# Kernel tuning notes

Measured on AMD Instinct MI355X. Metric: run time of the kernel, lower is better.

The kernel has to match this reference:

```python
import jax, jax.numpy as jnp
import numpy as np

MARGIN = 0.1
REDUCTION = 'mean'  # 'mean' or 'sum'

def setup_inputs() -> dict:
    key = jax.random.key(0)
    k1, k2 = jax.random.split(key)
    B, N = 16384, 64
    scores = jax.random.normal(k1, (B * N,), dtype=jnp.float32)
    werRank = jax.random.randint(k2, (B, N), 0, N, dtype=jnp.int64)
    return {"scores": scores, "werRank": werRank, "n_best": N}

def reference(scores, werRank, n_best):
    B = werRank.shape[0]
    N = n_best
    s = scores.reshape(B, N)                      # [B, N] per-utterance n-best scores
    g = jnp.take_along_axis(s, werRank, axis=1)   # [B, N] scores ordered by WER rank (best first)
    # pairwise margin: d[b, i, j] = g[b, j] - g[b, i] + margin, for worse-ranked j > i
    d = g[:, None, :] - g[:, :, None] + MARGIN    # [B, N, N]
    upper = jnp.triu(jnp.ones((N, N), dtype=bool), k=1)  # j > i
    hinge = jnp.where(upper[None], jnp.maximum(d, 0.0), 0.0)
    per_i = hinge.sum(axis=2)                     # [B, N] sum over worse hypotheses j
    if REDUCTION == 'mean':
        counts = (N - 1) - jnp.arange(N)          # len(nBestRank[i+1:]) for each i
        denom = jnp.where(counts > 0, counts, 1).astype(per_i.dtype)
        per_i = per_i / denom[None, :]            # row i=N-1 contributes 0 (skipped in original)
    return per_i.sum()
```

## Files before the change

### kernel.cpp

```cpp
#include <hip/hip_runtime.h>

#define MARGIN 0.1f
#define NBEST 64

__global__ __launch_bounds__(256)
void sml_kernel(const float* __restrict__ scores,
                const unsigned int* __restrict__ wr32,
                float* __restrict__ ws, int B)
{
    const int lane = threadIdx.x & 63;
    const int wib  = threadIdx.x >> 6;
    const int wgl  = blockIdx.x * 4 + wib;
    const int b0   = wgl * 4;

    unsigned int probe = wr32[2 * lane + 1];
    const bool is64 = (__all(probe == 0u) != 0);

    __shared__ float4 g4[4][NBEST];

    float gv[4];
    #pragma unroll
    for (int r = 0; r < 4; ++r) {
        int b  = b0 + r;
        int bc = (b < B) ? b : (B - 1);
        int idx = bc * NBEST + lane;
        unsigned int rk = is64 ? wr32[2 * idx] : wr32[idx];
        gv[r] = scores[bc * NBEST + (int)(rk & (NBEST - 1))];
    }
    float4 v = make_float4(gv[0], gv[1], gv[2], gv[3]);
    g4[wib][lane] = v;

    const float tx = MARGIN - v.x, ty = MARGIN - v.y;
    const float tz = MARGIN - v.z, tw = MARGIN - v.w;

    __syncthreads();

    float a0 = 0.0f, a1 = 0.0f, a2 = 0.0f, a3 = 0.0f;
    #pragma unroll
    for (int c = 0; c < NBEST; ++c) {
        float4 q = g4[wib][c];
        float m01 = (c > lane) ? 1.0f : 0.0f;
        a0 += fmaxf(q.x + tx, 0.0f) * m01;
        a1 += fmaxf(q.y + ty, 0.0f) * m01;
        a2 += fmaxf(q.z + tz, 0.0f) * m01;
        a3 += fmaxf(q.w + tw, 0.0f) * m01;
    }

    if (b0 + 1 >= B) a1 = 0.0f;
    if (b0 + 2 >= B) a2 = 0.0f;
    if (b0 + 3 >= B) a3 = 0.0f;
    if (b0 >= B)     a0 = 0.0f;

    int cnt = (NBEST - 1) - lane;
    float acc = (a0 + a1 + a2 + a3) / (float)(cnt > 0 ? cnt : 1);

    #pragma unroll
    for (int off = 32; off > 0; off >>= 1)
        acc += __shfl_down(acc, off);

    __shared__ float wsum[4];
    if (lane == 0) wsum[wib] = acc;
    __syncthreads();
    if (threadIdx.x == 0)
        ws[blockIdx.x] = wsum[0] + wsum[1] + wsum[2] + wsum[3];
}

__global__ __launch_bounds__(256)
void sml_reduce(const float* __restrict__ ws, float* __restrict__ out, int n)
{
    const int lane = threadIdx.x & 63;
    const int wid  = threadIdx.x >> 6;

    float s = 0.0f;
    for (int i = threadIdx.x; i < n; i += 256) s += ws[i];

    #pragma unroll
    for (int off = 32; off > 0; off >>= 1)
        s += __shfl_down(s, off);

    __shared__ float wsum[4];
    if (lane == 0) wsum[wid] = s;
    __syncthreads();
    if (threadIdx.x == 0)
        out[0] = wsum[0] + wsum[1] + wsum[2] + wsum[3];
}

extern "C" void kernel_launch(void* const* d_in, const int* in_sizes, int n_in,
                              void* d_out, int out_size, void* d_ws, size_t ws_size,
                              hipStream_t stream)
{
    const float* scores     = (const float*)d_in[0];
    const unsigned int* wr  = (const unsigned int*)d_in[1];
    const int B = in_sizes[0] / NBEST;

    const int blocks = (B + 15) / 16;
    sml_kernel<<<blocks, 256, 0, stream>>>(scores, wr, (float*)d_ws, B);
    sml_reduce<<<1, 256, 0, stream>>>((const float*)d_ws, (float*)d_out, blocks);
}
```

Measured before the change: 13.78 us.

## Broadcast scores via readlane and process eight rows per wave

Replaces the shared-memory float4 staging and __syncthreads with v_readlane broadcasts of each lane's gathered score. Each wave now handles eight rows instead of four, which halves the block count and the partial sums left for the reduce kernel. All index loads are issued before the score gathers so more memory requests are in flight at once. The cost is higher register pressure, fewer waves for such a small problem, and many scalar readlane instructions in the inner loop.

```diff
diff --git a/kernel.cpp b/kernel.cpp
--- a/kernel.cpp
+++ b/kernel.cpp
@@ -2,6 +2,7 @@
 
 #define MARGIN 0.1f
 #define NBEST 64
+#define ROWS_PER_WAVE 8
 
 __global__ __launch_bounds__(256)
 void sml_kernel(const float* __restrict__ scores,
@@ -10,49 +11,49 @@
 {
     const int lane = threadIdx.x & 63;
     const int wib  = threadIdx.x >> 6;
-    const int wgl  = blockIdx.x * 4 + wib;
-    const int b0   = wgl * 4;
+    const int b0   = (blockIdx.x * 4 + wib) * ROWS_PER_WAVE;
 
     unsigned int probe = wr32[2 * lane + 1];
     const bool is64 = (__all(probe == 0u) != 0);
 
-    __shared__ float4 g4[4][NBEST];
-
-    float gv[4];
+    unsigned int rk[ROWS_PER_WAVE];
     #pragma unroll
-    for (int r = 0; r < 4; ++r) {
-        int b  = b0 + r;
-        int bc = (b < B) ? b : (B - 1);
+    for (int r = 0; r < ROWS_PER_WAVE; ++r) {
+        int bc = min(b0 + r, B - 1);
         int idx = bc * NBEST + lane;
-        unsigned int rk = is64 ? wr32[2 * idx] : wr32[idx];
-        gv[r] = scores[bc * NBEST + (int)(rk & (NBEST - 1))];
+        rk[r] = is64 ? wr32[2 * idx] : wr32[idx];
     }
-    float4 v = make_float4(gv[0], gv[1], gv[2], gv[3]);
-    g4[wib][lane] = v;
-
-    const float tx = MARGIN - v.x, ty = MARGIN - v.y;
-    const float tz = MARGIN - v.z, tw = MARGIN - v.w;
-
-    __syncthreads();
-
-    float a0 = 0.0f, a1 = 0.0f, a2 = 0.0f, a3 = 0.0f;
+    float gv[ROWS_PER_WAVE];
     #pragma unroll
-    for (int c = 0; c < NBEST; ++c) {
-        float4 q = g4[wib][c];
-        float m01 = (c > lane) ? 1.0f : 0.0f;
-        a0 += fmaxf(q.x + tx, 0.0f) * m01;
-        a1 += fmaxf(q.y + ty, 0.0f) * m01;
-        a2 += fmaxf(q.z + tz, 0.0f) * m01;
-        a3 += fmaxf(q.w + tw, 0.0f) * m01;
+    for (int r = 0; r < ROWS_PER_WAVE; ++r) {
+        int bc = min(b0 + r, B - 1);
+        gv[r] = scores[bc * NBEST + (int)(rk[r] & (NBEST - 1))];
     }
 
-    if (b0 + 1 >= B) a1 = 0.0f;
-    if (b0 + 2 >= B) a2 = 0.0f;
-    if (b0 + 3 >= B) a3 = 0.0f;
-    if (b0 >= B)     a0 = 0.0f;
+    float t[ROWS_PER_WAVE], a[ROWS_PER_WAVE];
+    #pragma unroll
+    for (int r = 0; r < ROWS_PER_WAVE; ++r) {
+        t[r] = MARGIN - gv[r];
+        a[r] = 0.0f;
+    }
 
+    #pragma unroll
+    for (int c = 1; c < NBEST; ++c) {
+        float m01 = (lane < c) ? 1.0f : 0.0f;
+        #pragma unroll
+        for (int r = 0; r < ROWS_PER_WAVE; ++r) {
+            float s = __uint_as_float(
+                __builtin_amdgcn_readlane(__float_as_uint(gv[r]), c));
+            a[r] += fmaxf(s + t[r], 0.0f) * m01;
+        }
+    }
+
+    float accs = 0.0f;
+    #pragma unroll
+    for (int r = 0; r < ROWS_PER_WAVE; ++r)
+        accs += (b0 + r < B) ? a[r] : 0.0f;
     int cnt = (NBEST - 1) - lane;
-    float acc = (a0 + a1 + a2 + a3) / (float)(cnt > 0 ? cnt : 1);
+    float acc = accs / (float)(cnt > 0 ? cnt : 1);
 
     #pragma unroll
     for (int off = 32; off > 0; off >>= 1)
@@ -70,14 +71,11 @@
 {
     const int lane = threadIdx.x & 63;
     const int wid  = threadIdx.x >> 6;
-
     float s = 0.0f;
     for (int i = threadIdx.x; i < n; i += 256) s += ws[i];
-
     #pragma unroll
     for (int off = 32; off > 0; off >>= 1)
         s += __shfl_down(s, off);
-
     __shared__ float wsum[4];
     if (lane == 0) wsum[wid] = s;
     __syncthreads();
@@ -89,11 +87,12 @@
                               void* d_out, int out_size, void* d_ws, size_t ws_size,
                               hipStream_t stream)
 {
-    const float* scores     = (const float*)d_in[0];
-    const unsigned int* wr  = (const unsigned int*)d_in[1];
+    const float* scores    = (const float*)d_in[0];
+    const unsigned int* wr = (const unsigned int*)d_in[1];
     const int B = in_sizes[0] / NBEST;
 
-    const int blocks = (B + 15) / 16;
+    const int rows_per_block = 4 * ROWS_PER_WAVE;
+    const int blocks = (B + rows_per_block - 1) / rows_per_block;
     sml_kernel<<<blocks, 256, 0, stream>>>(scores, wr, (float*)d_ws, B);
     sml_reduce<<<1, 256, 0, stream>>>((const float*)d_ws, (float*)d_out, blocks);
 }
```

Result: slower. 16.12 us (+16.9%).
